# Performance work log

Measured on AMD Instinct MI355X. Metric: run time of the kernel, lower is better.

Reference implementation:

```python
import jax, jax.numpy as jnp
import numpy as np

K = 3        # kernel_size
STRIDE = 1
PAD = 1
OUT_H = 64
OUT_W = 64


def _unfold(x):
    """torch.nn.Unfold equivalent: x (B,C,H,W) -> patches (B, L, C*K*K),
    feature index ordered c*K*K + ki*K + kj (channel-major, like torch)."""
    B, C, H, W = x.shape
    xp = jnp.pad(x, ((0, 0), (0, 0), (PAD, PAD), (PAD, PAD)))
    # gather K*K shifted views; loop is over the small fixed kernel window only
    rows = []
    for ki in range(K):
        cols = []
        for kj in range(K):
            cols.append(xp[:, :, ki:ki + STRIDE * OUT_H:STRIDE,
                               kj:kj + STRIDE * OUT_W:STRIDE])  # (B,C,oh,ow)
        rows.append(jnp.stack(cols, axis=2))  # (B,C,K,oh,ow)
    p = jnp.stack(rows, axis=2)               # (B,C,K,K,oh,ow)
    # -> (B, oh, ow, C, K, K) -> (B, L, C*K*K)
    p = p.transpose(0, 4, 5, 1, 2, 3)
    return p.reshape(B, OUT_H * OUT_W, C * K * K)


def setup_inputs() -> dict:
    key = jax.random.key(0)
    k1, k2, k3 = jax.random.split(key, 3)
    B, C = 16, 32
    out_ch = 64
    L = OUT_H * OUT_W                 # 4096
    in_feat = C * K * K               # 288
    x = jax.random.normal(k1, (B, C, 64, 64), dtype=jnp.float32)
    # kaiming_uniform with a=sqrt(5) on (in_feat, out_ch) slices -> bound = 1/sqrt(in_feat)
    bound = 1.0 / np.sqrt(in_feat)
    weight = jax.random.uniform(k2, (L, in_feat, out_ch), dtype=jnp.float32,
                                minval=-bound, maxval=bound)
    bias = jax.random.uniform(k3, (L, out_ch), dtype=jnp.float32,
                              minval=-bound, maxval=bound)
    return {"x": x, "weight": weight, "bias": bias}


def reference(x, weight, bias):
    B = x.shape[0]
    out_ch = weight.shape[-1]
    patches = _unfold(x)                               # (B, L, in_feat)
    out = jnp.einsum('bli,lio->blo', patches, weight)  # per-location matmul
    out = out + bias[None]                             # (B, L, out_ch)
    out = out.transpose(0, 2, 1).reshape(B, out_ch, OUT_H, OUT_W)
    return out
```

## Files before the change

kernel.cpp:

```cpp
#include <hip/hip_runtime.h>

#define L_TOT   4096
#define CIN     32
#define G_L     4
#define CH      4
#define NCHUNK  24
#define CHUNK_STRIDE_F (CH * 3 * 64)

using f32g = __attribute__((address_space(1))) const float;
using f32l = __attribute__((address_space(3))) float;

#define FMA16(PP, WW) {                                                        \
    acc[0][0] += PP.x * WW.x; acc[0][1] += PP.x * WW.y;                        \
    acc[0][2] += PP.x * WW.z; acc[0][3] += PP.x * WW.w;                        \
    acc[1][0] += PP.y * WW.x; acc[1][1] += PP.y * WW.y;                        \
    acc[1][2] += PP.y * WW.z; acc[1][3] += PP.y * WW.w;                        \
    acc[2][0] += PP.z * WW.x; acc[2][1] += PP.z * WW.y;                        \
    acc[2][2] += PP.z * WW.z; acc[2][3] += PP.z * WW.w;                        \
    acc[3][0] += PP.w * WW.x; acc[3][1] += PP.w * WW.y;                        \
    acc[3][2] += PP.w * WW.z; acc[3][3] += PP.w * WW.w; }

#define COMPUTE4(K, WOFF) {                                                    \
    _Pragma("unroll")                                                          \
    for (int sl = 0; sl < CH; ++sl) {                                          \
        const int s = ((K) << 2) + sl;                                         \
        const float* pr = xs + ((6 * s + g) << 4) + (wv << 2);                 \
        float4 p0 = *(const float4*)(pr);                                      \
        float4 p1 = *(const float4*)(pr + 16);                                 \
        float4 p2 = *(const float4*)(pr + 32);                                 \
        const float4* wr = (const float4*)(&wsm[0][0] + (WOFF))                \
                           + g * 192 + sl * 48 + o4;                           \
        float4 w0 = wr[0];                                                     \
        float4 w1 = wr[16];                                                    \
        float4 w2 = wr[32];                                                    \
        FMA16(p0, w0); FMA16(p1, w1); FMA16(p2, w2);                           \
    } }

__global__ __launch_bounds__(256, 2)
void lc2d_v7(const float* __restrict__ x,
             const float* __restrict__ weight,
             const float* __restrict__ bias,
             float* __restrict__ out) {
    __shared__ __align__(16) float xs[576 * 16];
    __shared__ __align__(16) float wsm[3][12 * 256];

    const int tid  = threadIdx.x;
    const int lane = tid & 63;
    const int wv   = tid >> 6;
    const int g    = lane >> 4;
    const int o4   = lane & 15;

    const int bid  = blockIdx.x;
    const int swz  = ((bid & 7) << 7) | (bid >> 3);
    const int l0   = swz * G_L;
    const int oh   = l0 >> 6;
    const int ow0  = l0 & 63;

    const float* gsrc[3];
    int ldsoff[3];
#pragma unroll
    for (int t = 0; t < 3; ++t) {
        int p   = wv + (t << 2);
        int gg  = p / 3;
        int sub = p - 3 * gg;
        gsrc[t] = weight + (size_t)(l0 + gg) * (288 * 64) + sub * 256 + (lane << 2);
        ldsoff[t] = p * 256;
    }

#pragma unroll
    for (int t = 0; t < 3; ++t)
        __builtin_amdgcn_global_load_lds((f32g*)(gsrc[t]),
                                         (f32l*)(&wsm[0][ldsoff[t]]), 16, 0, 0);
#pragma unroll
    for (int t = 0; t < 3; ++t)
        __builtin_amdgcn_global_load_lds((f32g*)(gsrc[t] + CHUNK_STRIDE_F),
                                         (f32l*)(&wsm[1][ldsoff[t]]), 16, 0, 0);

    for (int u = tid; u < 1536; u += 256) {
        int b  = u & 15;
        int t  = u >> 4;
        int dh = t % 3;
        int c  = t / 3;
        int h  = oh - 1 + dh;
        bool hok = (unsigned)h < 64u;
        const float* xrow = x + (((b * CIN + c) * 64 + h) << 6);
        int wbase = ow0 - 1;
#pragma unroll
        for (int wl = 0; wl < 6; ++wl) {
            int ww = wbase + wl;
            float v = (hok && (unsigned)ww < 64u) ? xrow[ww] : 0.0f;
            xs[(t * 6 + wl) * 16 + b] = v;
        }
    }
    __syncthreads();

    const float4 bias4 = ((const float4*)bias)[(l0 + g) * 16 + o4];
    float acc[4][4];
#pragma unroll
    for (int bq = 0; bq < 4; ++bq) {
        acc[bq][0] = bias4.x; acc[bq][1] = bias4.y;
        acc[bq][2] = bias4.z; acc[bq][3] = bias4.w;
    }

    int wo0 = 0;
    int wo1 = 12 * 256;
    int wo2 = 2 * 12 * 256;
    for (int k = 0; k < NCHUNK - 2; ++k) {
#pragma unroll
        for (int t = 0; t < 3; ++t)
            __builtin_amdgcn_global_load_lds(
                (f32g*)(gsrc[t] + (size_t)(k + 2) * CHUNK_STRIDE_F),
                (f32l*)(&wsm[0][0] + wo2 + ldsoff[t]), 16, 0, 0);
        COMPUTE4(k, wo0);
        asm volatile("s_waitcnt vmcnt(3) lgkmcnt(0)" ::: "memory");
        __builtin_amdgcn_s_barrier();
        asm volatile("" ::: "memory");
        int tmp = wo0; wo0 = wo1; wo1 = wo2; wo2 = tmp;
    }
    COMPUTE4(NCHUNK - 2, wo0);
    asm volatile("s_waitcnt vmcnt(0) lgkmcnt(0)" ::: "memory");
    __builtin_amdgcn_s_barrier();
    asm volatile("" ::: "memory");
    COMPUTE4(NCHUNK - 1, wo1);

#pragma unroll
    for (int bq = 0; bq < 4; ++bq) {
        const int b = (wv << 2) + bq;
#pragma unroll
        for (int j = 0; j < 4; ++j) {
            out[((size_t)((b << 6) + (o4 << 2) + j) << 12) + l0 + g] = acc[bq][j];
        }
    }
}

extern "C" void kernel_launch(void* const* d_in, const int* in_sizes, int n_in,
                              void* d_out, int out_size, void* d_ws, size_t ws_size,
                              hipStream_t stream) {
    const float* x      = (const float*)d_in[0];
    const float* weight = (const float*)d_in[1];
    const float* bias   = (const float*)d_in[2];
    float* out          = (float*)d_out;

    dim3 grid(L_TOT / G_L);
    dim3 block(256);
    hipLaunchKernelGGL(lc2d_v7, grid, block, 0, stream, x, weight, bias, out);
}
```

Before: 442.9 us.

## Pre-transpose input to batch-innermost layout for vectorized patch loads

Adds a pre-pass kernel that rewrites x from (B,C,H,W) into a (C,H,W,B) workspace buffer, with the 16 batch entries contiguous. The main kernel then stages each patch row into LDS as float4 loads instead of scattered scalar loads. The aim is to cut the cost of the input-gather prologue. It adds an extra launch and an extra read and write of x, and it falls back to the old path when the workspace is too small.

```diff
diff --git a/kernel.cpp b/kernel.cpp
--- a/kernel.cpp
+++ b/kernel.cpp
@@ -6,9 +6,27 @@
 #define CH      4
 #define NCHUNK  24
 #define CHUNK_STRIDE_F (CH * 3 * 64)
+#define XT_FLOATS (32 * 64 * 64 * 16)
 
 using f32g = __attribute__((address_space(1))) const float;
 using f32l = __attribute__((address_space(3))) float;
+
+__global__ __launch_bounds__(256, 4)
+void xt_kernel(const float* __restrict__ x, float* __restrict__ xT) {
+    const int bi  = blockIdx.x;
+    const int c   = bi >> 6;
+    const int h   = bi & 63;
+    const int tid = threadIdx.x;
+    const int w   = tid >> 2;
+    const int bq  = tid & 3;
+    const int base = (((c << 6) + h) << 6) + w;
+    float4 v;
+    v.x = x[((bq << 2) + 0) * 131072 + base];
+    v.y = x[((bq << 2) + 1) * 131072 + base];
+    v.z = x[((bq << 2) + 2) * 131072 + base];
+    v.w = x[((bq << 2) + 3) * 131072 + base];
+    *(float4*)(xT + base * 16 + (bq << 2)) = v;
+}
 
 #define FMA16(PP, WW) {                                                        \
     acc[0][0] += PP.x * WW.x; acc[0][1] += PP.x * WW.y;                        \
@@ -36,8 +54,10 @@
         FMA16(p0, w0); FMA16(p1, w1); FMA16(p2, w2);                           \
     } }
 
+template <int USE_XT>
 __global__ __launch_bounds__(256, 2)
-void lc2d_v7(const float* __restrict__ x,
+void lc2d_v8(const float* __restrict__ x,
+             const float* __restrict__ xT,
              const float* __restrict__ weight,
              const float* __restrict__ bias,
              float* __restrict__ out) {
@@ -76,20 +96,39 @@
         __builtin_amdgcn_global_load_lds((f32g*)(gsrc[t] + CHUNK_STRIDE_F),
                                          (f32l*)(&wsm[1][ldsoff[t]]), 16, 0, 0);
 
-    for (int u = tid; u < 1536; u += 256) {
-        int b  = u & 15;
-        int t  = u >> 4;
-        int dh = t % 3;
-        int c  = t / 3;
-        int h  = oh - 1 + dh;
-        bool hok = (unsigned)h < 64u;
-        const float* xrow = x + (((b * CIN + c) * 64 + h) << 6);
-        int wbase = ow0 - 1;
+    if (USE_XT) {
 #pragma unroll
-        for (int wl = 0; wl < 6; ++wl) {
-            int ww = wbase + wl;
-            float v = (hok && (unsigned)ww < 64u) ? xrow[ww] : 0.0f;
-            xs[(t * 6 + wl) * 16 + b] = v;
+        for (int i = 0; i < 9; ++i) {
+            int e   = tid + (i << 8);
+            int b4  = e & 3;
+            int row = e >> 2;
+            int t   = row / 6;
+            int wl  = row - 6 * t;
+            int c   = t / 3;
+            int dh  = t - 3 * c;
+            int h   = oh - 1 + dh;
+            int ww  = ow0 - 1 + wl;
+            float4 v = {0.f, 0.f, 0.f, 0.f};
+            if (((unsigned)h < 64u) && ((unsigned)ww < 64u))
+                v = *(const float4*)(xT + ((((c << 6) + h) << 6) + ww) * 16 + (b4 << 2));
+            *(float4*)(&xs[(row << 4) + (b4 << 2)]) = v;
+        }
+    } else {
+        for (int u = tid; u < 1536; u += 256) {
+            int b  = u & 15;
+            int t  = u >> 4;
+            int dh = t % 3;
+            int c  = t / 3;
+            int h  = oh - 1 + dh;
+            bool hok = (unsigned)h < 64u;
+            const float* xrow = x + (((b * CIN + c) * 64 + h) << 6);
+            int wbase = ow0 - 1;
+#pragma unroll
+            for (int wl = 0; wl < 6; ++wl) {
+                int ww = wbase + wl;
+                float v = (hok && (unsigned)ww < 64u) ? xrow[ww] : 0.0f;
+                xs[(t * 6 + wl) * 16 + b] = v;
+            }
         }
     }
     __syncthreads();
@@ -141,7 +180,16 @@
     const float* bias   = (const float*)d_in[2];
     float* out          = (float*)d_out;
 
+    const size_t xt_bytes = (size_t)XT_FLOATS * 4;
     dim3 grid(L_TOT / G_L);
     dim3 block(256);
-    hipLaunchKernelGGL(lc2d_v7, grid, block, 0, stream, x, weight, bias, out);
+    if (d_ws != nullptr && ws_size >= xt_bytes) {
+        float* xT = (float*)d_ws;
+        hipLaunchKernelGGL(xt_kernel, dim3(32 * 64), dim3(256), 0, stream, x, xT);
+        hipLaunchKernelGGL((lc2d_v8<1>), grid, block, 0, stream,
+                           x, (const float*)xT, weight, bias, out);
+    } else {
+        hipLaunchKernelGGL((lc2d_v8<0>), grid, block, 0, stream,
+                           x, (const float*)nullptr, weight, bias, out);
+    }
 }
```

Measured after the change: 427.3 us. 3.5% less time.
